# Optimization experiments

Hardware: AMD Instinct MI355X
Metric: run time of the kernel (lower is better)

The kernel has to match this reference:

```python
import jax, jax.numpy as jnp
import numpy as np

E = 1024          # embed_dim
BS = 8            # number of sequences (bs = pre_lf_indexs.shape[0])
L = 8192          # tokens per sequence
N = BS * L        # packed tokens
CACHE = 16384     # lf cache rows
EPS = 1e-6


def setup_inputs() -> dict:
    key = jax.random.key(0)
    ks = jax.random.split(key, 9)
    inputs = jax.random.normal(ks[0], (N, E), jnp.float32)
    conv1_weight = jax.random.normal(ks[1], (E, E), jnp.float32) * (1.0 / np.sqrt(E))
    conv2_weight = jax.random.normal(ks[2], (E // 2, 2 * E), jnp.float32) * (1.0 / np.sqrt(E // 2))
    conv1_bias = jax.random.normal(ks[3], (E // 2,), jnp.float32) * 0.02
    conv2_bias = jax.random.normal(ks[4], (E,), jnp.float32) * 0.02
    ln_weight = jnp.ones((E,), jnp.float32)
    lf1_caches = jax.random.normal(ks[5], (CACHE, E), jnp.float32)
    lf2_caches = jax.random.normal(ks[6], (CACHE, E // 2), jnp.float32)
    # packed layout: each sequence prefixed by one cache slot -> T = N + BS rows
    offs = jnp.arange(BS, dtype=jnp.int32) * (L + 1)
    input_lf_loc = offs                                             # cache slot per seq
    inputs_loc = (offs[:, None] + 1 + jnp.arange(L, dtype=jnp.int32)[None, :]).reshape(-1)
    outputs_loc = inputs_loc - 1                                     # 2-tap causal pairing
    out_lf_loc = offs + L                                            # last token of each seq
    pre_lf_indexs = jax.random.randint(ks[7], (BS,), 0, CACHE, jnp.int32)
    out_lf_indexs = jax.random.randint(ks[8], (BS,), 0, CACHE, jnp.int32)
    return {
        'inputs': inputs, 'conv1_weight': conv1_weight, 'conv2_weight': conv2_weight,
        'conv1_bias': conv1_bias, 'conv2_bias': conv2_bias, 'ln_weight': ln_weight,
        'lf1_caches': lf1_caches, 'lf2_caches': lf2_caches,
        'pre_lf_indexs': pre_lf_indexs, 'out_lf_indexs': out_lf_indexs,
        'input_lf_loc': input_lf_loc, 'out_lf_loc': out_lf_loc,
        'inputs_loc': inputs_loc, 'outputs_loc': outputs_loc,
    }


def _fused_cat_conv2d(x, cache, W, pre_idx, in_lf_loc, in_loc, out_loc):
    # scatter cache rows + token rows into the padded buffer [N+bs, D]
    T = x.shape[0] + pre_idx.shape[0]
    xt = jnp.zeros((T, x.shape[1]), x.dtype)
    xt = xt.at[in_lf_loc].set(cache[pre_idx])   # gather from lf cache
    xt = xt.at[in_loc].set(x)
    co = xt @ W                                  # [T, 2*Dout]
    h = co.shape[1] // 2
    # shifted 2-tap causal conv: pair row j (prev) with row j+1 (cur)
    ot = co[:-1, :h] + co[1:, h:]                # [T-1, Dout]
    return ot[out_loc]                           # gather back to token order


def reference(inputs, conv1_weight, conv2_weight, conv1_bias, conv2_bias, ln_weight,
              lf1_caches, lf2_caches, pre_lf_indexs, out_lf_indexs,
              input_lf_loc, out_lf_loc, inputs_loc, outputs_loc):
    # (the index_put_ cache writes in the original are side effects for future
    #  steps only; they do not affect this call's output, so they are omitted)
    output1 = _fused_cat_conv2d(inputs, lf1_caches, conv1_weight,
                                pre_lf_indexs, input_lf_loc, inputs_loc, outputs_loc)
    output1 = output1 + conv1_bias               # [N, E/2]
    output2 = _fused_cat_conv2d(output1, lf2_caches, conv2_weight,
                                pre_lf_indexs, input_lf_loc, inputs_loc, outputs_loc)
    output2 = output2 + conv2_bias               # [N, E]
    x = output2 + inputs                         # residual
    var = jnp.mean(x * x, axis=-1, keepdims=True)
    return x * jax.lax.rsqrt(var + EPS) * ln_weight
```

## Files before the change

### kernel.cpp

```cpp
#include <hip/hip_runtime.h>
#include <hip/hip_bf16.h>


#define EDIM 1024
#define HDIM 512
#define LSEQ 8192
#define BSEQ 8
#define SEQR 8193
#define MTOT (BSEQ * SEQR)
#define MPAD 65792
#define XROWS 66048

using v8s = __attribute__((ext_vector_type(8))) short;
using v4f = __attribute__((ext_vector_type(4))) float;

__device__ __forceinline__ unsigned short f2b(float f) {
  union { float f; unsigned u; } v; v.f = f;
  unsigned r = v.u + 0x7fffu + ((v.u >> 16) & 1u);
  return (unsigned short)(r >> 16);
}
__device__ __forceinline__ float b2f(unsigned short h) {
  union { unsigned u; float f; } v; v.u = ((unsigned)h) << 16; return v.f;
}
__device__ __forceinline__ void gl_lds16(const void* g, void* l) {
  __builtin_amdgcn_global_load_lds((const __attribute__((address_space(1))) void*)g,
                                   (__attribute__((address_space(3))) void*)l, 16, 0, 0);
}

__global__ __launch_bounds__(256) void transpose_cat(const float* __restrict__ src, int src_ld,
                                                     int src_c0, unsigned short* __restrict__ dst,
                                                     int dst_ld, int dst_k0) {
  __shared__ float t[64][65];
  const int n0 = blockIdx.x * 64, k0 = blockIdx.y * 64;
  const int tx = threadIdx.x & 63, ty = threadIdx.x >> 6;
#pragma unroll
  for (int yy = 0; yy < 64; yy += 4)
    t[yy + ty][tx] = src[(size_t)(k0 + yy + ty) * src_ld + src_c0 + n0 + tx];
  __syncthreads();
#pragma unroll
  for (int yy = 0; yy < 64; yy += 4)
    dst[(size_t)(n0 + yy + ty) * dst_ld + dst_k0 + k0 + tx] = f2b(t[tx][yy + ty]);
}

__global__ void prep_small(const float* __restrict__ lf2, const int* __restrict__ preidx,
                           unsigned short* __restrict__ c2b) {
  const int tid = threadIdx.x;
#pragma unroll
  for (int b = 0; b < BSEQ; ++b)
    c2b[b * HDIM + tid] = f2b(lf2[(size_t)preidx[b] * HDIM + tid]);
}

__global__ __launch_bounds__(256) void cvt_full(const float* __restrict__ inputs,
                                                const float* __restrict__ lf1,
                                                const int* __restrict__ preidx,
                                                unsigned short* __restrict__ Xbf) {
  const int r = blockIdx.x * 4 + (threadIdx.x >> 6);
  const int lane = threadIdx.x & 63;
  unsigned short* dst = Xbf + (size_t)r * EDIM;
  if (r >= MTOT) {
#pragma unroll
    for (int c = lane * 4; c < EDIM; c += 256)
      *(ushort4*)&dst[c] = (ushort4){0, 0, 0, 0};
    return;
  }
  const int b = r / SEQR, rr = r % SEQR;
  const float* src = (rr == 0) ? (lf1 + (size_t)preidx[b] * EDIM)
                               : (inputs + (size_t)(b * LSEQ + rr - 1) * EDIM);
#pragma unroll
  for (int c = lane * 4; c < EDIM; c += 256) {
    const float4 v = *(const float4*)(src + c);
    *(ushort4*)&dst[c] = (ushort4){f2b(v.x), f2b(v.y), f2b(v.z), f2b(v.w)};
  }
}

__global__ void fixup_a2(const unsigned short* __restrict__ c2b,
                         unsigned short* __restrict__ A2) {
  const int tid = threadIdx.x;
#pragma unroll
  for (int b = 0; b < BSEQ; ++b)
    A2[(size_t)(b * SEQR) * HDIM + tid] = c2b[b * HDIM + tid];
}

#define PHASE(p, boA_)                                                                 \
  {                                                                                    \
    v8s af[2][2];                                                                      \
    _Pragma("unroll") for (int m2 = 0; m2 < 2; ++m2)                                   \
    _Pragma("unroll") for (int kx = 0; kx < 2; ++kx)                                   \
      af[m2][kx] = *(const v8s*)&lds[(boA_) + ((2 * (p) + m2) * 32 + wm * 16 + lr) * 64 + \
                                     (((kx * 4 + lk) ^ ra7) << 3)];                    \
    __builtin_amdgcn_s_setprio(1);                                                     \
    _Pragma("unroll") for (int m2 = 0; m2 < 2; ++m2)                                   \
    _Pragma("unroll") for (int nc = 0; nc < 4; ++nc)                                   \
    _Pragma("unroll") for (int kx = 0; kx < 2; ++kx)                                   \
      acc[2 * (p) + m2][nc] = __builtin_amdgcn_mfma_f32_16x16x32_bf16(                 \
          af[m2][kx], bf[nc][kx], acc[2 * (p) + m2][nc], 0, 0, 0);                     \
    __builtin_amdgcn_s_setprio(0);                                                     \
  }

#define LOAD_BFR(boB_)                                                                 \
  _Pragma("unroll") for (int nc = 0; nc < 4; ++nc)                                     \
  _Pragma("unroll") for (int kx = 0; kx < 2; ++kx)                                     \
    bf[nc][kx] = *(const v8s*)&lds[(boB_) + (nc * 64 + wn * 16 + lr) * 64 +            \
                                   (((kx * 4 + lk) ^ ra7) << 3)];

template <int K, int LDA, int NT, bool AMAP, bool SHIFTC>
__global__ __launch_bounds__(512, 2) void gemm3b(const unsigned short* __restrict__ A,
                                                 const unsigned short* __restrict__ B,
                                                 unsigned short* __restrict__ C,
                                                 const float* __restrict__ bias,
                                                 int q, int r) {
  __shared__ __align__(16) unsigned short lds[81920];
  constexpr int NTILES = K / 64;
  constexpr int N = NT * 256;
  const int h = blockIdx.x;
  const int xcd = h & 7, idx = h >> 3;
  const int tsw = (xcd < r ? xcd * (q + 1) : r * (q + 1) + (xcd - r) * q) + idx;
  const int mt = tsw / NT, nt = tsw % NT;
  const size_t m0 = (size_t)mt * 256, n0 = (size_t)nt * 256;
  const int tid = threadIdx.x;
  const int w = tid >> 6, lane = tid & 63;
  const int wm = w >> 2, wn = w & 3;
  const int lr = lane & 15, lk = lane >> 4;
  const int ra7 = lr & 7;
  const int srow = tid >> 3, slot = tid & 7;
  const int gslot = slot ^ (srow & 7);
  const int dA = srow * 64 + slot * 8;
  const unsigned short* bSrc = B + (size_t)(n0 + srow) * K + gslot * 8;

  auto stageA = [&](int dst, int hh, int tt) {
#pragma unroll
    for (int hf = 0; hf < 2; ++hf) {
      int u = (int)m0 + hh * 128 + hf * 64 + srow;
      if constexpr (AMAP) u += (u >> 13);
      gl_lds16(A + (size_t)u * LDA + tt * 64 + gslot * 8,
               &lds[dst + hh * 8192 + hf * 4096 + dA]);
    }
  };
  auto stageB = [&](int dst, int hh, int tt) {
    const unsigned short* s = bSrc + (size_t)hh * 128 * K + (size_t)tt * 64;
    unsigned short* d = &lds[dst + hh * 8192 + dA];
    gl_lds16(s, d);
    gl_lds16(s + (size_t)64 * K, d + 4096);
  };

  v4f acc[8][4];
#pragma unroll
  for (int i = 0; i < 8; ++i)
#pragma unroll
    for (int j = 0; j < 4; ++j) acc[i][j] = (v4f){0.f, 0.f, 0.f, 0.f};

  stageB(49152, 0, 0); stageB(49152, 1, 0);
  stageA(0, 0, 0);     stageA(0, 1, 0);
  stageA(16384, 0, 1); stageA(16384, 1, 1);
  asm volatile("s_waitcnt vmcnt(4)" ::: "memory");
  __builtin_amdgcn_s_barrier();

  int boA = 0, soA = 32768;
  int boB = 49152, sB = 65536;
#pragma unroll 1
  for (int t0 = 0; t0 < NTILES - 2; ++t0) {
    v8s bf[4][2];
    stageB(sB, 0, t0 + 1);
    LOAD_BFR(boB)
    PHASE(0, boA)
    stageB(sB, 1, t0 + 1);
    PHASE(1, boA)
    stageA(soA, 0, t0 + 2);
    PHASE(2, boA)
    stageA(soA, 1, t0 + 2);
    PHASE(3, boA)
    asm volatile("s_waitcnt vmcnt(4)" ::: "memory");
    __builtin_amdgcn_s_barrier();
    const int nboA = (boA == 32768) ? 0 : boA + 16384;
    soA = boA; boA = nboA;
    const int tmp = boB; boB = sB; sB = tmp;
  }
  {
    v8s bf[4][2];
    stageB(sB, 0, NTILES - 1);
    LOAD_BFR(boB)
    PHASE(0, boA)
    stageB(sB, 1, NTILES - 1);
    PHASE(1, boA)
    PHASE(2, boA)
    PHASE(3, boA)
    asm volatile("s_waitcnt vmcnt(0)" ::: "memory");
    __builtin_amdgcn_s_barrier();
    boA = (boA == 32768) ? 0 : boA + 16384;
    const int tmp = boB; boB = sB; sB = tmp;
  }
  {
    v8s bf[4][2];
    LOAD_BFR(boB)
    PHASE(0, boA) PHASE(1, boA) PHASE(2, boA) PHASE(3, boA)
  }

#pragma unroll
  for (int mr = 0; mr < 8; ++mr)
#pragma unroll
    for (int nc = 0; nc < 4; ++nc) {
      const size_t col = n0 + nc * 64 + wn * 16 + lr;
      float bv = 0.f;
      if constexpr (SHIFTC) bv = bias[col];
#pragma unroll
      for (int g = 0; g < 4; ++g) {
        const size_t row = m0 + mr * 32 + wm * 16 + lk * 4 + g + (SHIFTC ? 1 : 0);
        C[row * N + col] = f2b(acc[mr][nc][g] + bv);
      }
    }
}

__global__ __launch_bounds__(256) void epilogue_full(
    const unsigned short* __restrict__ Zo, const unsigned short* __restrict__ Xbf,
    const float* __restrict__ b2, const float* __restrict__ lnw,
    float* __restrict__ out) {
  const int u = blockIdx.x;
  const size_t rx = (size_t)u + (u >> 13) + 1;
  const int tid = threadIdx.x;
  const int j0 = tid * 4;

  const ushort4 z = *(const ushort4*)&Zo[(size_t)u * EDIM + j0];
  const ushort4 xb = *(const ushort4*)&Xbf[rx * EDIM + j0];
  const float4 bb = *(const float4*)&b2[j0];
  const float4 lw = *(const float4*)&lnw[j0];

  const float x0 = b2f(z.x) + bb.x + b2f(xb.x);
  const float x1 = b2f(z.y) + bb.y + b2f(xb.y);
  const float x2 = b2f(z.z) + bb.z + b2f(xb.z);
  const float x3 = b2f(z.w) + bb.w + b2f(xb.w);

  float ss = x0 * x0 + x1 * x1 + x2 * x2 + x3 * x3;
#pragma unroll
  for (int o = 32; o > 0; o >>= 1) ss += __shfl_xor(ss, o, 64);
  __shared__ float sp[4];
  if ((tid & 63) == 0) sp[tid >> 6] = ss;
  __syncthreads();
  const float tot = sp[0] + sp[1] + sp[2] + sp[3];
  const float scale = rsqrtf(tot * (1.0f / EDIM) + 1e-6f);

  float4 o4;
  o4.x = x0 * scale * lw.x; o4.y = x1 * scale * lw.y;
  o4.z = x2 * scale * lw.z; o4.w = x3 * scale * lw.w;
  *(float4*)&out[(size_t)u * EDIM + j0] = o4;
}

extern "C" void kernel_launch(void* const* d_in, const int* in_sizes, int n_in,
                              void* d_out, int out_size, void* d_ws, size_t ws_size,
                              hipStream_t stream) {
  const float* inputs = (const float*)d_in[0];
  const float* W1 = (const float*)d_in[1];
  const float* W2 = (const float*)d_in[2];
  const float* b1 = (const float*)d_in[3];
  const float* b2 = (const float*)d_in[4];
  const float* lnw = (const float*)d_in[5];
  const float* lf1 = (const float*)d_in[6];
  const float* lf2 = (const float*)d_in[7];
  const int* preidx = (const int*)d_in[8];
  float* out = (float*)d_out;

  char* ws = (char*)d_ws;
  unsigned short* Xbf = (unsigned short*)(ws);
  unsigned short* A2  = (unsigned short*)(ws + 135266304ULL);
  unsigned short* Zo  = (unsigned short*)(ws + 202899456ULL);
  unsigned short* W1c = (unsigned short*)(ws + 337117184ULL);
  unsigned short* W2c = (unsigned short*)(ws + 339214336ULL);
  unsigned short* c2b = (unsigned short*)(ws + 341311488ULL);

  transpose_cat<<<dim3(8, 16), 256, 0, stream>>>(W1, 1024, 0, W1c, 2048, 0);
  transpose_cat<<<dim3(8, 16), 256, 0, stream>>>(W1, 1024, 512, W1c, 2048, 1024);
  transpose_cat<<<dim3(16, 8), 256, 0, stream>>>(W2, 2048, 0, W2c, 1024, 0);
  transpose_cat<<<dim3(16, 8), 256, 0, stream>>>(W2, 2048, 1024, W2c, 1024, 512);
  prep_small<<<1, 512, 0, stream>>>(lf2, preidx, c2b);

  cvt_full<<<XROWS / 4, 256, 0, stream>>>(inputs, lf1, preidx, Xbf);
  gemm3b<2048, 1024, 2, false, true><<<514, 512, 0, stream>>>(Xbf, W1c, A2, b1, 64, 2);
  fixup_a2<<<1, 512, 0, stream>>>(c2b, A2);
  gemm3b<1024, 512, 4, true, false><<<1024, 512, 0, stream>>>(A2, W2c, Zo, nullptr, 128, 0);
  epilogue_full<<<BSEQ * LSEQ, 256, 0, stream>>>(Zo, Xbf, b2, lnw, out);
}
```

Baseline: 470.9 us.

## Restructure GEMM phase scheduling with barriers and handle GEMM1 tail rows separately

Rewrites the GEMM inner loop to preload A/B LDS fragments before each phase and wrap each MFMA phase in s_barrier plus sched_barrier, so the waves in a block issue their MFMA bursts in lockstep. Also shrinks the first GEMM grid from 514 to 512 blocks, giving an even split over the 8 XCDs, and computes the 7 leftover tail rows with a simple dot-product fixup kernel that also writes the cache rows. The extra barriers per phase add synchronisation overhead and may reduce latency hiding. The scalar fixup kernel is slow per row but only covers a few rows.

After: 498.9 us. 1.06x slower.

```diff
diff --git a/kernel.cpp b/kernel.cpp
--- a/kernel.cpp
+++ b/kernel.cpp
@@ -8,7 +8,6 @@
 #define BSEQ 8
 #define SEQR 8193
 #define MTOT (BSEQ * SEQR)
-#define MPAD 65792
 #define XROWS 66048
 
 using v8s = __attribute__((ext_vector_type(8))) short;
@@ -73,34 +72,57 @@
   }
 }
 
-__global__ void fixup_a2(const unsigned short* __restrict__ c2b,
-                         unsigned short* __restrict__ A2) {
+__global__ __launch_bounds__(512) void fixup_full(const unsigned short* __restrict__ Xbf,
+                                                  const unsigned short* __restrict__ W1c,
+                                                  const float* __restrict__ b1,
+                                                  const unsigned short* __restrict__ c2b,
+                                                  unsigned short* __restrict__ A2) {
+  const int blk = blockIdx.x;
   const int tid = threadIdx.x;
-#pragma unroll
-  for (int b = 0; b < BSEQ; ++b)
-    A2[(size_t)(b * SEQR) * HDIM + tid] = c2b[b * HDIM + tid];
-}
-
-#define PHASE(p, boA_)                                                                 \
-  {                                                                                    \
-    v8s af[2][2];                                                                      \
-    _Pragma("unroll") for (int m2 = 0; m2 < 2; ++m2)                                   \
-    _Pragma("unroll") for (int kx = 0; kx < 2; ++kx)                                   \
-      af[m2][kx] = *(const v8s*)&lds[(boA_) + ((2 * (p) + m2) * 32 + wm * 16 + lr) * 64 + \
-                                     (((kx * 4 + lk) ^ ra7) << 3)];                    \
-    __builtin_amdgcn_s_setprio(1);                                                     \
-    _Pragma("unroll") for (int m2 = 0; m2 < 2; ++m2)                                   \
-    _Pragma("unroll") for (int nc = 0; nc < 4; ++nc)                                   \
-    _Pragma("unroll") for (int kx = 0; kx < 2; ++kx)                                   \
-      acc[2 * (p) + m2][nc] = __builtin_amdgcn_mfma_f32_16x16x32_bf16(                 \
-          af[m2][kx], bf[nc][kx], acc[2 * (p) + m2][nc], 0, 0, 0);                     \
-    __builtin_amdgcn_s_setprio(0);                                                     \
-  }
-
-#define LOAD_BFR(boB_)                                                                 \
-  _Pragma("unroll") for (int nc = 0; nc < 4; ++nc)                                     \
-  _Pragma("unroll") for (int kx = 0; kx < 2; ++kx)                                     \
-    bf[nc][kx] = *(const v8s*)&lds[(boB_) + (nc * 64 + wn * 16 + lr) * 64 +            \
+  if (blk == 7) {
+#pragma unroll
+    for (int b = 0; b < BSEQ; ++b)
+      A2[(size_t)(b * SEQR) * HDIM + tid] = c2b[b * HDIM + tid];
+    return;
+  }
+  const int r = 65536 + blk;
+  const unsigned short* a = Xbf + (size_t)r * EDIM;
+  const unsigned short* wrow = W1c + (size_t)tid * 2048;
+  float s = 0.f;
+  for (int k = 0; k < 2048; k += 8) {
+    const v8s av = *(const v8s*)&a[k];
+    const v8s wv = *(const v8s*)&wrow[k];
+#pragma unroll
+    for (int j = 0; j < 8; ++j)
+      s += b2f((unsigned short)av[j]) * b2f((unsigned short)wv[j]);
+  }
+  A2[(size_t)(r + 1) * HDIM + tid] = f2b(s + b1[tid]);
+}
+
+#define LOAD_AFR(p)                                                                   \
+  _Pragma("unroll") for (int m2 = 0; m2 < 2; ++m2)                                    \
+  _Pragma("unroll") for (int kx = 0; kx < 2; ++kx)                                    \
+    af[m2][kx] = *(const v8s*)&lds[boA + ((2 * (p) + m2) * 32 + wm * 16 + lr) * 64 +  \
+                                   (((kx * 4 + lk) ^ ra7) << 3)];
+
+#define PHASE_SYNC_MFMA(p)                                                            \
+  __builtin_amdgcn_s_barrier();                                                       \
+  asm volatile("s_waitcnt lgkmcnt(0)" ::: "memory");                                  \
+  __builtin_amdgcn_sched_barrier(0);                                                  \
+  __builtin_amdgcn_s_setprio(1);                                                      \
+  _Pragma("unroll") for (int m2 = 0; m2 < 2; ++m2)                                    \
+  _Pragma("unroll") for (int nc = 0; nc < 4; ++nc)                                    \
+  _Pragma("unroll") for (int kx = 0; kx < 2; ++kx)                                    \
+    acc[2 * (p) + m2][nc] = __builtin_amdgcn_mfma_f32_16x16x32_bf16(                  \
+        af[m2][kx], bf[nc][kx], acc[2 * (p) + m2][nc], 0, 0, 0);                      \
+  __builtin_amdgcn_s_setprio(0);                                                      \
+  __builtin_amdgcn_sched_barrier(0);                                                  \
+  __builtin_amdgcn_s_barrier();
+
+#define LOAD_BFR()                                                                    \
+  _Pragma("unroll") for (int nc = 0; nc < 4; ++nc)                                    \
+  _Pragma("unroll") for (int kx = 0; kx < 2; ++kx)                                    \
+    bf[nc][kx] = *(const v8s*)&lds[boB + (nc * 64 + wn * 16 + lr) * 64 +              \
                                    (((kx * 4 + lk) ^ ra7) << 3)];
 
 template <int K, int LDA, int NT, bool AMAP, bool SHIFTC>
@@ -159,40 +181,53 @@
   int boB = 49152, sB = 65536;
 #pragma unroll 1
   for (int t0 = 0; t0 < NTILES - 2; ++t0) {
-    v8s bf[4][2];
+    v8s bf[4][2], af[2][2];
+    LOAD_BFR()
+    LOAD_AFR(0)
     stageB(sB, 0, t0 + 1);
-    LOAD_BFR(boB)
-    PHASE(0, boA)
+    PHASE_SYNC_MFMA(0)
+    LOAD_AFR(1)
     stageB(sB, 1, t0 + 1);
-    PHASE(1, boA)
+    PHASE_SYNC_MFMA(1)
+    LOAD_AFR(2)
     stageA(soA, 0, t0 + 2);
-    PHASE(2, boA)
+    PHASE_SYNC_MFMA(2)
+    LOAD_AFR(3)
     stageA(soA, 1, t0 + 2);
-    PHASE(3, boA)
     asm volatile("s_waitcnt vmcnt(4)" ::: "memory");
-    __builtin_amdgcn_s_barrier();
+    PHASE_SYNC_MFMA(3)
     const int nboA = (boA == 32768) ? 0 : boA + 16384;
     soA = boA; boA = nboA;
     const int tmp = boB; boB = sB; sB = tmp;
   }
   {
-    v8s bf[4][2];
+    v8s bf[4][2], af[2][2];
+    LOAD_BFR()
+    LOAD_AFR(0)
     stageB(sB, 0, NTILES - 1);
-    LOAD_BFR(boB)
-    PHASE(0, boA)
+    PHASE_SYNC_MFMA(0)
+    LOAD_AFR(1)
     stageB(sB, 1, NTILES - 1);
-    PHASE(1, boA)
-    PHASE(2, boA)
-    PHASE(3, boA)
+    PHASE_SYNC_MFMA(1)
+    LOAD_AFR(2)
+    PHASE_SYNC_MFMA(2)
+    LOAD_AFR(3)
     asm volatile("s_waitcnt vmcnt(0)" ::: "memory");
-    __builtin_amdgcn_s_barrier();
+    PHASE_SYNC_MFMA(3)
     boA = (boA == 32768) ? 0 : boA + 16384;
     const int tmp = boB; boB = sB; sB = tmp;
   }
   {
-    v8s bf[4][2];
-    LOAD_BFR(boB)
-    PHASE(0, boA) PHASE(1, boA) PHASE(2, boA) PHASE(3, boA)
+    v8s bf[4][2], af[2][2];
+    LOAD_BFR()
+    LOAD_AFR(0)
+    PHASE_SYNC_MFMA(0)
+    LOAD_AFR(1)
+    PHASE_SYNC_MFMA(1)
+    LOAD_AFR(2)
+    PHASE_SYNC_MFMA(2)
+    LOAD_AFR(3)
+    PHASE_SYNC_MFMA(3)
   }
 
 #pragma unroll
@@ -273,8 +308,8 @@
   prep_small<<<1, 512, 0, stream>>>(lf2, preidx, c2b);
 
   cvt_full<<<XROWS / 4, 256, 0, stream>>>(inputs, lf1, preidx, Xbf);
-  gemm3b<2048, 1024, 2, false, true><<<514, 512, 0, stream>>>(Xbf, W1c, A2, b1, 64, 2);
-  fixup_a2<<<1, 512, 0, stream>>>(c2b, A2);
+  gemm3b<2048, 1024, 2, false, true><<<512, 512, 0, stream>>>(Xbf, W1c, A2, b1, 64, 0);
+  fixup_full<<<8, 512, 0, stream>>>(Xbf, W1c, b1, c2b, A2);
   gemm3b<1024, 512, 4, true, false><<<1024, 512, 0, stream>>>(A2, W2c, Zo, nullptr, 128, 0);
   epilogue_full<<<BSEQ * LSEQ, 256, 0, stream>>>(Zo, Xbf, b2, lnw, out);
 }
```

## Fuse bias and residual into second GEMM epilogue; trim first GEMM tail tiles

Applied to the files above, without the earlier changes.

The second GEMM epilogue now adds the conv2 bias and the bf16 residual input before storing. This leaves the final kernel to do only the RMS normalisation, and it no longer reads Xbf or the bias. The first GEMM launches 512 blocks instead of 514, dropping the two padded tail tiles. The seven leftover rows are computed by a small scalar dot-product kernel that also performs the old cache-row fixup. The residual reads in the GEMM epilogue are strided per lane, and the tail rows now run on a slow scalar path.

New measurement: 503.2 us. 1.07x slower.

```diff
diff --git a/kernel.cpp b/kernel.cpp
--- a/kernel.cpp
+++ b/kernel.cpp
@@ -8,7 +8,6 @@
 #define BSEQ 8
 #define SEQR 8193
 #define MTOT (BSEQ * SEQR)
-#define MPAD 65792
 #define XROWS 66048
 
 using v8s = __attribute__((ext_vector_type(8))) short;
@@ -73,12 +72,31 @@
   }
 }
 
-__global__ void fixup_a2(const unsigned short* __restrict__ c2b,
-                         unsigned short* __restrict__ A2) {
-  const int tid = threadIdx.x;
-#pragma unroll
-  for (int b = 0; b < BSEQ; ++b)
-    A2[(size_t)(b * SEQR) * HDIM + tid] = c2b[b * HDIM + tid];
+__global__ __launch_bounds__(512) void fixup_full(const unsigned short* __restrict__ Xbf,
+                                                  const unsigned short* __restrict__ W1c,
+                                                  const float* __restrict__ b1,
+                                                  const unsigned short* __restrict__ c2b,
+                                                  unsigned short* __restrict__ A2) {
+  const int blk = blockIdx.x;
+  const int tid = threadIdx.x;
+  if (blk == 7) {
+#pragma unroll
+    for (int b = 0; b < BSEQ; ++b)
+      A2[(size_t)(b * SEQR) * HDIM + tid] = c2b[b * HDIM + tid];
+    return;
+  }
+  const int r = 65536 + blk;
+  const unsigned short* a = Xbf + (size_t)r * EDIM;
+  const unsigned short* wrow = W1c + (size_t)tid * 2048;
+  float s = 0.f;
+  for (int k = 0; k < 2048; k += 8) {
+    const v8s av = *(const v8s*)&a[k];
+    const v8s wv = *(const v8s*)&wrow[k];
+#pragma unroll
+    for (int j = 0; j < 8; ++j)
+      s += b2f((unsigned short)av[j]) * b2f((unsigned short)wv[j]);
+  }
+  A2[(size_t)(r + 1) * HDIM + tid] = f2b(s + b1[tid]);
 }
 
 #define PHASE(p, boA_)                                                                 \
@@ -103,11 +121,12 @@
     bf[nc][kx] = *(const v8s*)&lds[(boB_) + (nc * 64 + wn * 16 + lr) * 64 +            \
                                    (((kx * 4 + lk) ^ ra7) << 3)];
 
-template <int K, int LDA, int NT, bool AMAP, bool SHIFTC>
+template <int K, int LDA, int NT, bool AMAP, bool SHIFTC, bool RESID>
 __global__ __launch_bounds__(512, 2) void gemm3b(const unsigned short* __restrict__ A,
                                                  const unsigned short* __restrict__ B,
                                                  unsigned short* __restrict__ C,
                                                  const float* __restrict__ bias,
+                                                 const unsigned short* __restrict__ Xres,
                                                  int q, int r) {
   __shared__ __align__(16) unsigned short lds[81920];
   constexpr int NTILES = K / 64;
@@ -201,33 +220,31 @@
     for (int nc = 0; nc < 4; ++nc) {
       const size_t col = n0 + nc * 64 + wn * 16 + lr;
       float bv = 0.f;
-      if constexpr (SHIFTC) bv = bias[col];
+      if constexpr (SHIFTC || RESID) bv = bias[col];
 #pragma unroll
       for (int g = 0; g < 4; ++g) {
-        const size_t row = m0 + mr * 32 + wm * 16 + lk * 4 + g + (SHIFTC ? 1 : 0);
-        C[row * N + col] = f2b(acc[mr][nc][g] + bv);
+        const size_t row = m0 + mr * 32 + wm * 16 + lk * 4 + g;
+        if constexpr (RESID) {
+          const size_t rx = row + (row >> 13) + 1;
+          const float x = acc[mr][nc][g] + bv + b2f(Xres[rx * EDIM + col]);
+          C[row * N + col] = f2b(x);
+        } else {
+          C[(row + (SHIFTC ? 1 : 0)) * N + col] = f2b(acc[mr][nc][g] + bv);
+        }
       }
     }
 }
 
-__global__ __launch_bounds__(256) void epilogue_full(
-    const unsigned short* __restrict__ Zo, const unsigned short* __restrict__ Xbf,
-    const float* __restrict__ b2, const float* __restrict__ lnw,
-    float* __restrict__ out) {
+__global__ __launch_bounds__(256) void rms_final(const unsigned short* __restrict__ Zo,
+                                                 const float* __restrict__ lnw,
+                                                 float* __restrict__ out) {
   const int u = blockIdx.x;
-  const size_t rx = (size_t)u + (u >> 13) + 1;
   const int tid = threadIdx.x;
   const int j0 = tid * 4;
 
   const ushort4 z = *(const ushort4*)&Zo[(size_t)u * EDIM + j0];
-  const ushort4 xb = *(const ushort4*)&Xbf[rx * EDIM + j0];
-  const float4 bb = *(const float4*)&b2[j0];
   const float4 lw = *(const float4*)&lnw[j0];
-
-  const float x0 = b2f(z.x) + bb.x + b2f(xb.x);
-  const float x1 = b2f(z.y) + bb.y + b2f(xb.y);
-  const float x2 = b2f(z.z) + bb.z + b2f(xb.z);
-  const float x3 = b2f(z.w) + bb.w + b2f(xb.w);
+  const float x0 = b2f(z.x), x1 = b2f(z.y), x2 = b2f(z.z), x3 = b2f(z.w);
 
   float ss = x0 * x0 + x1 * x1 + x2 * x2 + x3 * x3;
 #pragma unroll
@@ -273,8 +290,10 @@
   prep_small<<<1, 512, 0, stream>>>(lf2, preidx, c2b);
 
   cvt_full<<<XROWS / 4, 256, 0, stream>>>(inputs, lf1, preidx, Xbf);
-  gemm3b<2048, 1024, 2, false, true><<<514, 512, 0, stream>>>(Xbf, W1c, A2, b1, 64, 2);
-  fixup_a2<<<1, 512, 0, stream>>>(c2b, A2);
-  gemm3b<1024, 512, 4, true, false><<<1024, 512, 0, stream>>>(A2, W2c, Zo, nullptr, 128, 0);
-  epilogue_full<<<BSEQ * LSEQ, 256, 0, stream>>>(Zo, Xbf, b2, lnw, out);
-}
+  gemm3b<2048, 1024, 2, false, true, false>
+      <<<512, 512, 0, stream>>>(Xbf, W1c, A2, b1, nullptr, 64, 0);
+  fixup_full<<<8, 512, 0, stream>>>(Xbf, W1c, b1, c2b, A2);
+  gemm3b<1024, 512, 4, true, false, true>
+      <<<1024, 512, 0, stream>>>(A2, W2c, Zo, b2, Xbf, 128, 0);
+  rms_final<<<BSEQ * LSEQ, 256, 0, stream>>>(Zo, lnw, out);
+}
```

## Reuse shared A tile across both conv taps and merge prep launches

Applied to the files above, without the earlier changes.

The 2-tap GEMM now stages a 257-row A tile once per 64-wide K chunk and reuses it for both taps: the second tap reads the same LDS tile shifted by one row. Before, the concatenated K=2*D operand was reloaded, so this roughly halves A global traffic and LDS fill. The first GEMM drops from 514 to 512 blocks, and the leftover tail rows are computed by a scalar dot-product fixup kernel. The four weight transposes and the cache-row conversion are merged into one launch to cut launch overhead. The reworked pipeline uses a different barrier and waitcnt schedule and has correctness risk around the shifted swizzle and tail rows.

Measured after the change: 471.5 us. Within noise of the previous version (+0.1%).

```diff
diff --git a/kernel.cpp b/kernel.cpp
--- a/kernel.cpp
+++ b/kernel.cpp
@@ -8,7 +8,6 @@
 #define BSEQ 8
 #define SEQR 8193
 #define MTOT (BSEQ * SEQR)
-#define MPAD 65792
 #define XROWS 66048
 
 using v8s = __attribute__((ext_vector_type(8))) short;
@@ -27,12 +26,9 @@
                                    (__attribute__((address_space(3))) void*)l, 16, 0, 0);
 }
 
-__global__ __launch_bounds__(256) void transpose_cat(const float* __restrict__ src, int src_ld,
-                                                     int src_c0, unsigned short* __restrict__ dst,
-                                                     int dst_ld, int dst_k0) {
-  __shared__ float t[64][65];
-  const int n0 = blockIdx.x * 64, k0 = blockIdx.y * 64;
-  const int tx = threadIdx.x & 63, ty = threadIdx.x >> 6;
+__device__ __forceinline__ void trns64(const float* __restrict__ src, int src_ld, int src_c0,
+                                       unsigned short* __restrict__ dst, int dst_ld, int dst_k0,
+                                       int n0, int k0, float (*t)[65], int tx, int ty) {
 #pragma unroll
   for (int yy = 0; yy < 64; yy += 4)
     t[yy + ty][tx] = src[(size_t)(k0 + yy + ty) * src_ld + src_c0 + n0 + tx];
@@ -42,12 +38,29 @@
     dst[(size_t)(n0 + yy + ty) * dst_ld + dst_k0 + k0 + tx] = f2b(t[tx][yy + ty]);
 }
 
-__global__ void prep_small(const float* __restrict__ lf2, const int* __restrict__ preidx,
-                           unsigned short* __restrict__ c2b) {
+__global__ __launch_bounds__(256) void prep_all(const float* __restrict__ W1,
+                                                const float* __restrict__ W2,
+                                                const float* __restrict__ lf2,
+                                                const int* __restrict__ preidx,
+                                                unsigned short* __restrict__ W1c,
+                                                unsigned short* __restrict__ W2c,
+                                                unsigned short* __restrict__ c2b) {
+  __shared__ float t[64][65];
+  const int bk = blockIdx.x;
   const int tid = threadIdx.x;
-#pragma unroll
-  for (int b = 0; b < BSEQ; ++b)
-    c2b[b * HDIM + tid] = f2b(lf2[(size_t)preidx[b] * HDIM + tid]);
+  if (bk == 512) {
+    for (int c = tid; c < HDIM; c += 256)
+#pragma unroll
+      for (int b = 0; b < BSEQ; ++b)
+        c2b[b * HDIM + c] = f2b(lf2[(size_t)preidx[b] * HDIM + c]);
+    return;
+  }
+  const int tx = tid & 63, ty = tid >> 6;
+  const int which = bk >> 7, s = bk & 127;
+  if (which == 0)       trns64(W1, 1024, 0,    W1c, 2048, 0,    (s & 7) * 64,  (s >> 3) * 64, t, tx, ty);
+  else if (which == 1)  trns64(W1, 1024, 512,  W1c, 2048, 1024, (s & 7) * 64,  (s >> 3) * 64, t, tx, ty);
+  else if (which == 2)  trns64(W2, 2048, 0,    W2c, 1024, 0,    (s & 15) * 64, (s >> 4) * 64, t, tx, ty);
+  else                  trns64(W2, 2048, 1024, W2c, 1024, 512,  (s & 15) * 64, (s >> 4) * 64, t, tx, ty);
 }
 
 __global__ __launch_bounds__(256) void cvt_full(const float* __restrict__ inputs,
@@ -73,21 +86,41 @@
   }
 }
 
-__global__ void fixup_a2(const unsigned short* __restrict__ c2b,
-                         unsigned short* __restrict__ A2) {
+__global__ __launch_bounds__(512) void fixup_full(const unsigned short* __restrict__ Xbf,
+                                                  const unsigned short* __restrict__ W1c,
+                                                  const float* __restrict__ b1,
+                                                  const unsigned short* __restrict__ c2b,
+                                                  unsigned short* __restrict__ A2) {
+  const int blk = blockIdx.x;
   const int tid = threadIdx.x;
-#pragma unroll
-  for (int b = 0; b < BSEQ; ++b)
-    A2[(size_t)(b * SEQR) * HDIM + tid] = c2b[b * HDIM + tid];
-}
-
-#define PHASE(p, boA_)                                                                 \
+  if (blk == 7) {
+#pragma unroll
+    for (int b = 0; b < BSEQ; ++b)
+      A2[(size_t)(b * SEQR) * HDIM + tid] = c2b[b * HDIM + tid];
+    return;
+  }
+  const int r = 65536 + blk;
+  const unsigned short* a = Xbf + (size_t)r * EDIM;
+  const unsigned short* wrow = W1c + (size_t)tid * 2048;
+  float s = 0.f;
+  for (int k = 0; k < 2048; k += 8) {
+    const v8s av = *(const v8s*)&a[k];
+    const v8s wv = *(const v8s*)&wrow[k];
+#pragma unroll
+    for (int j = 0; j < 8; ++j)
+      s += b2f((unsigned short)av[j]) * b2f((unsigned short)wv[j]);
+  }
+  A2[(size_t)(r + 1) * HDIM + tid] = f2b(s + b1[tid]);
+}
+
+#define PHASE(p, boA_, off_, ra_)                                                      \
   {                                                                                    \
     v8s af[2][2];                                                                      \
     _Pragma("unroll") for (int m2 = 0; m2 < 2; ++m2)                                   \
     _Pragma("unroll") for (int kx = 0; kx < 2; ++kx)                                   \
-      af[m2][kx] = *(const v8s*)&lds[(boA_) + ((2 * (p) + m2) * 32 + wm * 16 + lr) * 64 + \
-                                     (((kx * 4 + lk) ^ ra7) << 3)];                    \
+      af[m2][kx] = *(const v8s*)&lds[(boA_) +                                          \
+          ((2 * (p) + m2) * 32 + wm * 16 + lr + (off_)) * 64 +                         \
+          (((kx * 4 + lk) ^ (ra_)) << 3)];                                             \
     __builtin_amdgcn_s_setprio(1);                                                     \
     _Pragma("unroll") for (int m2 = 0; m2 < 2; ++m2)                                   \
     _Pragma("unroll") for (int nc = 0; nc < 4; ++nc)                                   \
@@ -101,17 +134,24 @@
   _Pragma("unroll") for (int nc = 0; nc < 4; ++nc)                                     \
   _Pragma("unroll") for (int kx = 0; kx < 2; ++kx)                                     \
     bf[nc][kx] = *(const v8s*)&lds[(boB_) + (nc * 64 + wn * 16 + lr) * 64 +            \
-                                   (((kx * 4 + lk) ^ ra7) << 3)];
-
-template <int K, int LDA, int NT, bool AMAP, bool SHIFTC>
-__global__ __launch_bounds__(512, 2) void gemm3b(const unsigned short* __restrict__ A,
-                                                 const unsigned short* __restrict__ B,
-                                                 unsigned short* __restrict__ C,
-                                                 const float* __restrict__ bias,
-                                                 int q, int r) {
-  __shared__ __align__(16) unsigned short lds[81920];
-  constexpr int NTILES = K / 64;
+                                   (((kx * 4 + lk) ^ ra7a) << 3)];
+
+#define STEP4(boA_, off_, ra_)                                                         \
+  PHASE(0, boA_, off_, ra_) PHASE(1, boA_, off_, ra_)                                  \
+  PHASE(2, boA_, off_, ra_) PHASE(3, boA_, off_, ra_)
+
+template <int K, int NT, bool SHIFTC, bool AMAP>
+__global__ __launch_bounds__(512, 2) void gemm_pair(const unsigned short* __restrict__ A,
+                                                    const unsigned short* __restrict__ B,
+                                                    unsigned short* __restrict__ C,
+                                                    const float* __restrict__ bias,
+                                                    int q, int r) {
+  constexpr int NH = K / 128;
+  constexpr int LDA = K / 2;
   constexpr int N = NT * 256;
+  constexpr int A0 = 0, A1 = 16512, B_A = 33024, B_B = 49408;
+  __shared__ __align__(16) unsigned short lds[65792];
+
   const int h = blockIdx.x;
   const int xcd = h & 7, idx = h >> 3;
   const int tsw = (xcd < r ? xcd * (q + 1) : r * (q + 1) + (xcd - r) * q) + idx;
@@ -121,24 +161,26 @@
   const int w = tid >> 6, lane = tid & 63;
   const int wm = w >> 2, wn = w & 3;
   const int lr = lane & 15, lk = lane >> 4;
-  const int ra7 = lr & 7;
+  const int ra7a = lr & 7, ra7b = (lr + 1) & 7;
   const int srow = tid >> 3, slot = tid & 7;
   const int gslot = slot ^ (srow & 7);
-  const int dA = srow * 64 + slot * 8;
-  const unsigned short* bSrc = B + (size_t)(n0 + srow) * K + gslot * 8;
-
-  auto stageA = [&](int dst, int hh, int tt) {
-#pragma unroll
-    for (int hf = 0; hf < 2; ++hf) {
-      int u = (int)m0 + hh * 128 + hf * 64 + srow;
-      if constexpr (AMAP) u += (u >> 13);
-      gl_lds16(A + (size_t)u * LDA + tt * 64 + gslot * 8,
-               &lds[dst + hh * 8192 + hf * 4096 + dA]);
+  const int dAB = srow * 64 + slot * 8;
+  const int aBase = (int)m0 + (AMAP ? ((int)m0 >> 13) : 0);
+
+  auto stageApair = [&](int dstE, int i) {
+#pragma unroll
+    for (int j = 0; j < 4; ++j) {
+      const int rr = j * 64 + (tid >> 3);
+      gl_lds16(A + (size_t)(aBase + rr) * LDA + i * 64 + ((tid & 7) ^ (rr & 7)) * 8,
+               &lds[dstE + rr * 64 + (tid & 7) * 8]);
     }
+    if (tid < 8)
+      gl_lds16(A + (size_t)(aBase + 256) * LDA + i * 64 + tid * 8,
+               &lds[dstE + 256 * 64 + tid * 8]);
   };
-  auto stageB = [&](int dst, int hh, int tt) {
-    const unsigned short* s = bSrc + (size_t)hh * 128 * K + (size_t)tt * 64;
-    unsigned short* d = &lds[dst + hh * 8192 + dA];
+  auto stageB = [&](int dstE, int hh, int t) {
+    const unsigned short* s = B + (size_t)(n0 + hh * 128 + srow) * K + t * 64 + gslot * 8;
+    unsigned short* d = &lds[dstE + hh * 8192 + dAB];
     gl_lds16(s, d);
     gl_lds16(s + (size_t)64 * K, d + 4096);
   };
@@ -149,50 +191,38 @@
 #pragma unroll
     for (int j = 0; j < 4; ++j) acc[i][j] = (v4f){0.f, 0.f, 0.f, 0.f};
 
-  stageB(49152, 0, 0); stageB(49152, 1, 0);
-  stageA(0, 0, 0);     stageA(0, 1, 0);
-  stageA(16384, 0, 1); stageA(16384, 1, 1);
-  asm volatile("s_waitcnt vmcnt(4)" ::: "memory");
+  stageApair(A0, 0);
+  stageB(B_A, 0, 0); stageB(B_A, 1, 0);
+  asm volatile("s_waitcnt vmcnt(0)" ::: "memory");
   __builtin_amdgcn_s_barrier();
 
-  int boA = 0, soA = 32768;
-  int boB = 49152, sB = 65536;
 #pragma unroll 1
-  for (int t0 = 0; t0 < NTILES - 2; ++t0) {
+  for (int i = 0; i < NH - 1; ++i) {
+    const int boA = (i & 1) ? A1 : A0;
+    const int soA = (i & 1) ? A0 : A1;
     v8s bf[4][2];
-    stageB(sB, 0, t0 + 1);
-    LOAD_BFR(boB)
-    PHASE(0, boA)
-    stageB(sB, 1, t0 + 1);
-    PHASE(1, boA)
-    stageA(soA, 0, t0 + 2);
-    PHASE(2, boA)
-    stageA(soA, 1, t0 + 2);
-    PHASE(3, boA)
+    stageB(B_B, 0, i + NH); stageB(B_B, 1, i + NH);
+    stageApair(soA, i + 1);
+    LOAD_BFR(B_A)
+    STEP4(boA, 0, ra7a)
     asm volatile("s_waitcnt vmcnt(4)" ::: "memory");
     __builtin_amdgcn_s_barrier();
-    const int nboA = (boA == 32768) ? 0 : boA + 16384;
-    soA = boA; boA = nboA;
-    const int tmp = boB; boB = sB; sB = tmp;
-  }
-  {
-    v8s bf[4][2];
-    stageB(sB, 0, NTILES - 1);
-    LOAD_BFR(boB)
-    PHASE(0, boA)
-    stageB(sB, 1, NTILES - 1);
-    PHASE(1, boA)
-    PHASE(2, boA)
-    PHASE(3, boA)
+    stageB(B_A, 0, i + 1); stageB(B_A, 1, i + 1);
+    LOAD_BFR(B_B)
+    STEP4(boA, 1, ra7b)
     asm volatile("s_waitcnt vmcnt(0)" ::: "memory");
     __builtin_amdgcn_s_barrier();
-    boA = (boA == 32768) ? 0 : boA + 16384;
-    const int tmp = boB; boB = sB; sB = tmp;
   }
   {
+    const int boA = ((NH - 1) & 1) ? A1 : A0;
     v8s bf[4][2];
-    LOAD_BFR(boB)
-    PHASE(0, boA) PHASE(1, boA) PHASE(2, boA) PHASE(3, boA)
+    stageB(B_B, 0, 2 * NH - 1); stageB(B_B, 1, 2 * NH - 1);
+    LOAD_BFR(B_A)
+    STEP4(boA, 0, ra7a)
+    asm volatile("s_waitcnt vmcnt(0)" ::: "memory");
+    __builtin_amdgcn_s_barrier();
+    LOAD_BFR(B_B)
+    STEP4(boA, 1, ra7b)
   }
 
 #pragma unroll
@@ -266,15 +296,10 @@
   unsigned short* W2c = (unsigned short*)(ws + 339214336ULL);
   unsigned short* c2b = (unsigned short*)(ws + 341311488ULL);
 
-  transpose_cat<<<dim3(8, 16), 256, 0, stream>>>(W1, 1024, 0, W1c, 2048, 0);
-  transpose_cat<<<dim3(8, 16), 256, 0, stream>>>(W1, 1024, 512, W1c, 2048, 1024);
-  transpose_cat<<<dim3(16, 8), 256, 0, stream>>>(W2, 2048, 0, W2c, 1024, 0);
-  transpose_cat<<<dim3(16, 8), 256, 0, stream>>>(W2, 2048, 1024, W2c, 1024, 512);
-  prep_small<<<1, 512, 0, stream>>>(lf2, preidx, c2b);
-
+  prep_all<<<513, 256, 0, stream>>>(W1, W2, lf2, preidx, W1c, W2c, c2b);
   cvt_full<<<XROWS / 4, 256, 0, stream>>>(inputs, lf1, preidx, Xbf);
-  gemm3b<2048, 1024, 2, false, true><<<514, 512, 0, stream>>>(Xbf, W1c, A2, b1, 64, 2);
-  fixup_a2<<<1, 512, 0, stream>>>(c2b, A2);
-  gemm3b<1024, 512, 4, true, false><<<1024, 512, 0, stream>>>(A2, W2c, Zo, nullptr, 128, 0);
+  gemm_pair<2048, 2, true, false><<<512, 512, 0, stream>>>(Xbf, W1c, A2, b1, 64, 0);
+  fixup_full<<<8, 512, 0, stream>>>(Xbf, W1c, b1, c2b, A2);
+  gemm_pair<1024, 4, false, true><<<1024, 512, 0, stream>>>(A2, W2c, Zo, nullptr, 128, 0);
   epilogue_full<<<BSEQ * LSEQ, 256, 0, stream>>>(Zo, Xbf, b2, lnw, out);
 }
```
